# Kernel tuning notes

Hardware: AMD Instinct MI355X
Metric: run time of the kernel (lower is better)

## Reference

```python
import jax, jax.numpy as jnp
import numpy as np

# CompositionBlock math, exploiting the dependency-tree sparsity exactly.
# Original torch module builds dense [B,S,S,*] tensors, but after masking only
# pairs (i=head[j], j) carry the true bilinear value; every other pair carries
# tanh(0)=0 into the composition bilinear, yielding the constant tanh(b_comp).
# The final Linear(S,1) reduces over j, so:
#   out[b,i,t] = sum_j Wr[j]*tanh(b_comp)[t] + b_red
#              + sum_{j: head[b,j]==i} Wr[j]*(special[b,j,t] - tanh(b_comp)[t])
# where special[b,j] = tanh(Bilinear2(tok[b,j], tanh(Bilinear1(tok[b,j], dep[b,j])))).
# This is bit-identical math to the dense masked version (in exact arithmetic).

B, S, T, D, P = 8, 256, 128, 64, 128

def setup_inputs() -> dict:
    key = jax.random.key(0)
    ks = jax.random.split(key, 9)
    return {
        "token_embeddings": jax.random.normal(ks[0], (B, S, T), jnp.float32),
        "dep_embeddings": jax.random.normal(ks[1], (B, S, D), jnp.float32),
        "dep_heads": jax.random.randint(ks[2], (B, S), 0, S + 1),  # S == root/no-head
        "W_dep": jax.random.normal(ks[3], (P, T, D), jnp.float32) * 0.05,   # Bilinear1 weight [out,in1,in2]
        "b_dep": jax.random.normal(ks[4], (P,), jnp.float32) * 0.05,
        "W_comp": jax.random.normal(ks[5], (T, T, P), jnp.float32) * 0.05,  # Bilinear2 weight
        "b_comp": jax.random.normal(ks[6], (T,), jnp.float32) * 0.05,
        "W_red": jax.random.normal(ks[7], (1, S), jnp.float32) * 0.05,      # Linear(S,1) weight
        "b_red": jax.random.normal(ks[8], (1,), jnp.float32) * 0.05,
    }

def reference(token_embeddings, dep_embeddings, dep_heads,
              W_dep, b_dep, W_comp, b_comp, W_red, b_red):
    Bb, Ss, Tt = token_embeddings.shape
    # Bilinear1 per token pair-with-self (only diagonal j is ever used): [B,S,P]
    tde = jnp.einsum('bjt,ptd,bjd->bjp', token_embeddings, W_dep, dep_embeddings) + b_dep
    # Valid-edge composition value: [B,S,T]
    special = jnp.tanh(
        jnp.einsum('bjt,otp,bjp->bjo', token_embeddings, W_comp, jnp.tanh(tde)) + b_comp
    )
    base = jnp.tanh(b_comp)            # value at all masked-out (invalid) pairs, [T]
    wr = W_red[0]                      # [S], reduction weights over j
    # one_hot maps j -> its head i; out-of-range head (== S, the root) -> all zeros
    onehot = jax.nn.one_hot(dep_heads, Ss, dtype=token_embeddings.dtype)  # [B,j,i]
    out = (jnp.einsum('bji,j,bjt->bit', onehot, wr, special - base)
           + base * jnp.sum(wr) + b_red[0])                               # [B,S,T]
    return out
```

## Files before the change

### kernel.cpp

```cpp
#include <hip/hip_runtime.h>
#include <cstdint>
#include <cstddef>

#define Bsz 8
#define Ssz 256
#define Msz 2048
#define SPLITK 16

typedef _Float16 f16x8 __attribute__((ext_vector_type(8)));
typedef _Float16 f16x4 __attribute__((ext_vector_type(4)));
typedef float f32x16 __attribute__((ext_vector_type(16)));

__global__ __launch_bounds__(256) void k_pack(
    const float* __restrict__ W1, const float* __restrict__ W2,
    const float* __restrict__ dep, const float* __restrict__ tok,
    _Float16* __restrict__ W1pk, _Float16* __restrict__ W2pk,
    _Float16* __restrict__ dpk,  _Float16* __restrict__ tokT)
{
  __shared__ float tile[32][33];
  const int bx = blockIdx.x, tid = threadIdx.x;
  if (bx < 768) {
    const bool isW1 = bx < 256;
    const int idx = (isW1 ? bx : bx - 256) * 256 + tid;
    const int r  = idx & 31;
    const int pb = (idx >> 5) & 3;
    const int kc = idx >> 7;
    const float* src = (isW1 ? W1 : W2) + (size_t)(pb * 32 + r) * (isW1 ? 8192 : 16384) + kc * 16;
    const float4* s4 = (const float4*)src;
    float4 u0 = s4[0], u1 = s4[1], u2 = s4[2], u3 = s4[3];
    f16x8 lo = {(_Float16)u0.x,(_Float16)u0.y,(_Float16)u0.z,(_Float16)u0.w,
                (_Float16)u1.x,(_Float16)u1.y,(_Float16)u1.z,(_Float16)u1.w};
    f16x8 hi = {(_Float16)u2.x,(_Float16)u2.y,(_Float16)u2.z,(_Float16)u2.w,
                (_Float16)u3.x,(_Float16)u3.y,(_Float16)u3.z,(_Float16)u3.w};
    _Float16* dst = (isW1 ? W1pk : W2pk) + ((size_t)(kc * 4 + pb) * 64) * 8;
    *(f16x8*)(dst + (size_t)r * 8)        = lo;
    *(f16x8*)(dst + (size_t)(32 + r) * 8) = hi;
  } else if (bx < 832) {
    const int idx = (bx - 768) * 256 + tid;
    const int m = idx & 2047, pc = idx >> 11;
    const float4* s4 = (const float4*)(dep + (size_t)m * 64 + pc * 8);
    float4 u0 = s4[0], u1 = s4[1];
    f16x8 v = {(_Float16)u0.x,(_Float16)u0.y,(_Float16)u0.z,(_Float16)u0.w,
               (_Float16)u1.x,(_Float16)u1.y,(_Float16)u1.z,(_Float16)u1.w};
    *(f16x8*)(dpk + ((size_t)pc * Msz + m) * 8) = v;
  } else {
    const int q = bx - 832;
    const int mt = q >> 2, tt = q & 3;
    const int tx = tid & 31, ty = tid >> 5;
    for (int yy = ty; yy < 32; yy += 8)
      tile[yy][tx] = tok[(size_t)(mt * 32 + yy) * 128 + tt * 32 + tx];
    __syncthreads();
    for (int yy = ty; yy < 32; yy += 8)
      tokT[(size_t)(tt * 32 + yy) * Msz + mt * 32 + tx] = (_Float16)tile[tx][yy];
  }
}

template<int LGDV, int KC>
__global__ __launch_bounds__(512, 4) void k_gemm(
    const _Float16* __restrict__ Apk,
    const _Float16* __restrict__ Wpk,
    const _Float16* __restrict__ tokT,
    float* __restrict__ part)
{
  constexpr int DV  = 1 << LGDV;
  constexpr int NT  = KC >> LGDV;
  constexpr int NKS = DV >> 4;

  const int tid  = threadIdx.x;
  const int lane = tid & 63;
  const int wv   = tid >> 6;
  const int wm   = wv >> 2;
  const int wo   = wv & 3;
  const int l31  = lane & 31;
  const int lg   = lane >> 5;
  const int id   = blockIdx.x;
  const int sk   = (id & 7) + 8 * (id >> 8);
  const int mb   = (id >> 3) & 31;
  const int m0   = mb * 64;
  const int mrow0 = m0 + wm * 32 + l31;

  f16x8 a[NKS];
  #pragma unroll
  for (int ks = 0; ks < NKS; ++ks)
    a[ks] = *(const f16x8*)(Apk + ((size_t)(ks * 2 + lg) * Msz + mrow0) * 8);

  const int t0 = sk * NT;
  _Float16 tr[NT];
  #pragma unroll
  for (int i = 0; i < NT; ++i)
    tr[i] = tokT[(size_t)(t0 + i) * Msz + mrow0];

  f32x16 acc = {};
  const int kc0 = sk * (KC >> 4);

  #pragma unroll
  for (int tg = 0; tg < NT; ++tg) {
    const _Float16 ta = tr[tg];
    const f16x8 tav = {ta,ta,ta,ta,ta,ta,ta,ta};
    #pragma unroll
    for (int ks = 0; ks < NKS; ++ks) {
      const f16x8 b = *(const f16x8*)(Wpk + (((size_t)(kc0 + tg * NKS + ks) * 4 + wo) * 64 + lane) * 8);
      const f16x8 af = tav * a[ks];
      acc = __builtin_amdgcn_mfma_f32_32x32x16_f16(af, b, acc, 0, 0, 0);
    }
  }

  float* dst = part + (size_t)sk * Msz * 128;
  const int ocol = wo * 32 + l31;
  #pragma unroll
  for (int r = 0; r < 16; ++r) {
    const int mrow = m0 + wm * 32 + (r & 3) + 8 * (r >> 2) + 4 * lg;
    dst[(size_t)mrow * 128 + ocol] = acc[r];
  }
}

template<bool TO_HPK>
__global__ __launch_bounds__(256) void k_red(
    const float* __restrict__ part, const float* __restrict__ bias,
    _Float16* __restrict__ hpk, float* __restrict__ spc)
{
  const int u  = blockIdx.x * 256 + threadIdx.x;
  const int e4 = u * 4;
  const int m = e4 >> 7, p = e4 & 127;
  float4 s = *(const float4*)(bias + p);
  #pragma unroll
  for (int sk = 0; sk < SPLITK; sk++) {
    float4 v = *(const float4*)(part + (size_t)sk * (Msz * 128) + e4);
    s.x += v.x; s.y += v.y; s.z += v.z; s.w += v.w;
  }
  s.x = tanhf(s.x); s.y = tanhf(s.y); s.z = tanhf(s.z); s.w = tanhf(s.w);
  if (TO_HPK) {
    f16x4 h4 = {(_Float16)s.x, (_Float16)s.y, (_Float16)s.z, (_Float16)s.w};
    *(f16x4*)(hpk + ((size_t)(p >> 3) * Msz + m) * 8 + (p & 7)) = h4;
  } else {
    *(float4*)(spc + e4) = s;
  }
}

__global__ __launch_bounds__(128) void k_finalize(
    const float* __restrict__ special,
    const int*   __restrict__ heads,
    const float* __restrict__ wred,
    const float* __restrict__ bred,
    const float* __restrict__ bcomp,
    float* __restrict__ out)
{
  int b = blockIdx.x >> 8;
  int i = blockIdx.x & 255;
  int t = threadIdx.x;
  __shared__ float wr_s[Ssz];
  __shared__ int   hd_s[Ssz];
  wr_s[t]       = wred[t];
  wr_s[t + 128] = wred[t + 128];
  hd_s[t]       = heads[b * Ssz + t];
  hd_s[t + 128] = heads[b * Ssz + t + 128];
  __syncthreads();

  const float base  = tanhf(bcomp[t]);
  const float bred0 = bred[0];
  float swr = 0.f, accv = 0.f;
  #pragma unroll 1
  for (int j = 0; j < Ssz; j++) {
    swr += wr_s[j];
    if (hd_s[j] == i)
      accv += wr_s[j] * (special[((size_t)b * Ssz + j) * 128 + t] - base);
  }
  out[((size_t)b * Ssz + i) * 128 + t] = base * swr + bred0 + accv;
}

extern "C" void kernel_launch(void* const* d_in, const int* in_sizes, int n_in,
                              void* d_out, int out_size, void* d_ws, size_t ws_size,
                              hipStream_t stream) {
  const float* tok   = (const float*)d_in[0];
  const float* dep   = (const float*)d_in[1];
  const int*   hds   = (const int*)  d_in[2];
  const float* Wdep  = (const float*)d_in[3];
  const float* bdep  = (const float*)d_in[4];
  const float* Wcomp = (const float*)d_in[5];
  const float* bcomp = (const float*)d_in[6];
  const float* Wred  = (const float*)d_in[7];
  const float* bred  = (const float*)d_in[8];
  float* out = (float*)d_out;

  char* ws = (char*)d_ws;
  _Float16* W1pk = (_Float16*)(ws);
  _Float16* W2pk = (_Float16*)(ws + (2u  << 20));
  _Float16* dpk  = (_Float16*)(ws + (6u  << 20));
  _Float16* tokT = (_Float16*)(ws + (7u  << 20));
  _Float16* hpk  = (_Float16*)(ws + (8u  << 20));
  float*    part = (float*)   (ws + (9u  << 20));
  float*    spc  = (float*)   (ws + (25u << 20));

  k_pack<<<1088, 256, 0, stream>>>(Wdep, Wcomp, dep, tok, W1pk, W2pk, dpk, tokT);

  k_gemm<6, 512><<<512, 512, 0, stream>>>(dpk, W1pk, tokT, part);
  k_red<true><<<256, 256, 0, stream>>>(part, bdep, hpk, nullptr);

  k_gemm<7, 1024><<<512, 512, 0, stream>>>(hpk, W2pk, tokT, part);
  k_red<false><<<256, 256, 0, stream>>>(part, bcomp, nullptr, spc);

  k_finalize<<<dim3(Bsz * Ssz), 128, 0, stream>>>(spc, hds, Wred, bred, bcomp, out);
}
```

Measured before the change: 73.10 us.

## Retile GEMM so each wave computes two output tiles sharing A fragments

The split-K GEMM kernels now give each block 128 rows instead of 64, and each wave computes a 32x64 output tile (two MFMA accumulators) instead of 32x32. The scaled A fragment is reused across two B fragments, halving A loads and the tav*a multiplies per MFMA. The grid drops from 512 to 256 blocks, and launch bounds relax to 2 blocks per CU to allow more registers. Fewer blocks on a large GPU may leave compute units idle.

```diff
diff --git a/kernel.cpp b/kernel.cpp
--- a/kernel.cpp
+++ b/kernel.cpp
@@ -56,7 +56,7 @@
 }
 
 template<int LGDV, int KC>
-__global__ __launch_bounds__(512, 4) void k_gemm(
+__global__ __launch_bounds__(512, 2) void k_gemm(
     const _Float16* __restrict__ Apk,
     const _Float16* __restrict__ Wpk,
     const _Float16* __restrict__ tokT,
@@ -69,14 +69,12 @@
   const int tid  = threadIdx.x;
   const int lane = tid & 63;
   const int wv   = tid >> 6;
-  const int wm   = wv >> 2;
-  const int wo   = wv & 3;
+  const int wm   = wv >> 1;
+  const int wn   = wv & 1;
   const int l31  = lane & 31;
   const int lg   = lane >> 5;
-  const int id   = blockIdx.x;
-  const int sk   = (id & 7) + 8 * (id >> 8);
-  const int mb   = (id >> 3) & 31;
-  const int m0   = mb * 64;
+  const int m0   = blockIdx.x * 128;
+  const int sk   = blockIdx.y;
   const int mrow0 = m0 + wm * 32 + l31;
 
   f16x8 a[NKS];
@@ -85,32 +83,35 @@
     a[ks] = *(const f16x8*)(Apk + ((size_t)(ks * 2 + lg) * Msz + mrow0) * 8);
 
   const int t0 = sk * NT;
-  _Float16 tr[NT];
+  _Float16 tra[NT];
   #pragma unroll
   for (int i = 0; i < NT; ++i)
-    tr[i] = tokT[(size_t)(t0 + i) * Msz + mrow0];
-
-  f32x16 acc = {};
+    tra[i] = tokT[(size_t)(t0 + i) * Msz + mrow0];
+
+  f32x16 acc0 = {}, acc1 = {};
   const int kc0 = sk * (KC >> 4);
-
   #pragma unroll
   for (int tg = 0; tg < NT; ++tg) {
-    const _Float16 ta = tr[tg];
+    const _Float16 ta = tra[tg];
     const f16x8 tav = {ta,ta,ta,ta,ta,ta,ta,ta};
     #pragma unroll
     for (int ks = 0; ks < NKS; ++ks) {
-      const f16x8 b = *(const f16x8*)(Wpk + (((size_t)(kc0 + tg * NKS + ks) * 4 + wo) * 64 + lane) * 8);
+      const _Float16* bp = Wpk + (((size_t)(kc0 + tg * NKS + ks) * 4 + wn * 2) * 64 + lane) * 8;
+      const f16x8 b0 = *(const f16x8*)(bp);
+      const f16x8 b1 = *(const f16x8*)(bp + 64 * 8);
       const f16x8 af = tav * a[ks];
-      acc = __builtin_amdgcn_mfma_f32_32x32x16_f16(af, b, acc, 0, 0, 0);
+      acc0 = __builtin_amdgcn_mfma_f32_32x32x16_f16(af, b0, acc0, 0, 0, 0);
+      acc1 = __builtin_amdgcn_mfma_f32_32x32x16_f16(af, b1, acc1, 0, 0, 0);
     }
   }
 
-  float* dst = part + (size_t)sk * Msz * 128;
-  const int ocol = wo * 32 + l31;
+  float* dst = part + (size_t)sk * (Msz * 128);
+  const int col0 = wn * 64 + l31;
   #pragma unroll
   for (int r = 0; r < 16; ++r) {
     const int mrow = m0 + wm * 32 + (r & 3) + 8 * (r >> 2) + 4 * lg;
-    dst[(size_t)mrow * 128 + ocol] = acc[r];
+    dst[(size_t)mrow * 128 + col0]      = acc0[r];
+    dst[(size_t)mrow * 128 + col0 + 32] = acc1[r];
   }
 }
 
@@ -193,10 +194,10 @@
 
   k_pack<<<1088, 256, 0, stream>>>(Wdep, Wcomp, dep, tok, W1pk, W2pk, dpk, tokT);
 
-  k_gemm<6, 512><<<512, 512, 0, stream>>>(dpk, W1pk, tokT, part);
+  k_gemm<6, 512><<<dim3(16, SPLITK), 512, 0, stream>>>(dpk, W1pk, tokT, part);
   k_red<true><<<256, 256, 0, stream>>>(part, bdep, hpk, nullptr);
 
-  k_gemm<7, 1024><<<512, 512, 0, stream>>>(hpk, W2pk, tokT, part);
+  k_gemm<7, 1024><<<dim3(16, SPLITK), 512, 0, stream>>>(hpk, W2pk, tokT, part);
   k_red<false><<<256, 256, 0, stream>>>(part, bcomp, nullptr, spc);
 
   k_finalize<<<dim3(Bsz * Ssz), 128, 0, stream>>>(spc, hds, Wred, bred, bcomp, out);
```

New measurement: 68.51 us. 6.3% less time.
